# Kernel tuning notes

Measured on AMD Instinct MI355X. Metric: run time of the kernel, lower is better.

Reference implementation:

```python
import jax, jax.numpy as jnp
import numpy as np

WINDOW_SIZE = 7
L = 255.0
C1 = (0.01 * L) ** 2
C2 = (0.03 * L) ** 2


def _box_filter(x, window):
    # x: [B,1,H,W], window: [1,1,k,k] (uniform 1/k^2). VALID conv, groups=1.
    return jax.lax.conv_general_dilated(
        x, window, window_strides=(1, 1), padding='VALID',
        dimension_numbers=('NCHW', 'OIHW', 'NCHW'))


def setup_inputs() -> dict:
    key = jax.random.key(0)
    k1, k2 = jax.random.split(key)
    shape = (16, 1, 1080, 1920)
    img1 = jax.random.uniform(k1, shape, dtype=jnp.float32) * L
    img2 = jax.random.uniform(k2, shape, dtype=jnp.float32) * L
    window = jnp.ones((1, 1, WINDOW_SIZE, WINDOW_SIZE), dtype=jnp.float32) / (WINDOW_SIZE * WINDOW_SIZE)
    return {"img1": img1, "img2": img2, "window": window}


def reference(img1, img2, window):
    mu1 = _box_filter(img1, window)
    mu2 = _box_filter(img2, window)
    mu1_sq = mu1 * mu1
    mu2_sq = mu2 * mu2
    mu1_mu2 = mu1 * mu2
    sigma1_sq = _box_filter(img1 * img1, window) - mu1_sq
    sigma2_sq = _box_filter(img2 * img2, window) - mu2_sq
    sigma12 = _box_filter(img1 * img2, window) - mu1_mu2
    v1 = 2.0 * sigma12 + C2
    v2 = sigma1_sq + sigma2_sq + C2
    ssim_map = (2.0 * mu1_mu2 + C1) * v1 / ((mu1_sq + mu2_sq + C1) * v2)
    return jnp.mean(ssim_map)
```

## Files before the change

kernel.cpp:

```cpp
#include <hip/hip_runtime.h>


constexpr int W_IN = 1920;
constexpr int H_IN = 1080;
constexpr int WOUT = W_IN - 6;
constexpr int HOUT = H_IN - 6;
constexpr int NBATCH = 16;

constexpr int TW = 256;
constexpr int TH = 64;
constexpr int SROWS = 7;
constexpr int NSTAGES = 10;
constexpr int LSTRIDE = 264;
constexpr int C4_PER_ROW = 66;
constexpr int TASKS_PER_IMG = SROWS * C4_PER_ROW;
constexpr int TASKS = 2 * TASKS_PER_IMG;
constexpr int IMG_OFF = SROWS * LSTRIDE;
constexpr int BUF_OFF = 2 * IMG_OFF;

constexpr int NBX = 8, NBY = 17;
constexpr int NBLOCKS = NBX * NBY * NBATCH;

constexpr float C1f = 6.5025f;
constexpr float C2f = 58.5225f;
constexpr float INV49 = 1.0f / 49.0f;

__global__ __launch_bounds__(256)
void ssim_kernel(const float* __restrict__ img1, const float* __restrict__ img2,
                 double* __restrict__ partial) {
  const int tid = threadIdx.x;
  const int x0 = blockIdx.x * TW;
  const int y0 = blockIdx.y * TH;
  const size_t ibase = (size_t)blockIdx.z * (size_t)(H_IN * W_IN);
  const float* __restrict__ b1p = img1 + ibase;
  const float* __restrict__ b2p = img2 + ibase;

  __shared__ float sh[2 * BUF_OFF];
  __shared__ float warpsum[4];

#define DECODE(K)                                                        \
  const int  i##K  = tid + (K)*256;                                      \
  const bool v##K  = i##K < TASKS;                                       \
  const int  im##K = (i##K >= TASKS_PER_IMG) ? 1 : 0;                    \
  const int  rm##K = i##K - im##K * TASKS_PER_IMG;                       \
  const int  r##K  = rm##K / C4_PER_ROW;                                 \
  const int  c##K  = rm##K - r##K * C4_PER_ROW;                          \
  const int  gx##K = min(x0 + c##K * 4, W_IN - 4);                       \
  const float* pb##K = (im##K ? b2p : b1p) + gx##K;                      \
  const int  ld##K = (im##K * SROWS + r##K) * LSTRIDE + c##K * 4;
  DECODE(0) DECODE(1) DECODE(2) DECODE(3)
#undef DECODE

  float4 g0, g1, g2, g3;
#define GLOAD(K, ROW0)                                                   \
  if (v##K) {                                                            \
    const int gy = min(y0 + (ROW0) + r##K, H_IN - 1);                    \
    g##K = *reinterpret_cast<const float4*>(pb##K + (size_t)gy * W_IN);  \
  }
#define SWRITE(K, BUFBASE)                                               \
  if (v##K) *reinterpret_cast<float4*>(sh + (BUFBASE) + ld##K) = g##K;

#define DECL_SLOT(J) float h1_##J, h2_##J, h11_##J, h22_##J, h12_##J;
  DECL_SLOT(0) DECL_SLOT(1) DECL_SLOT(2) DECL_SLOT(3)
  DECL_SLOT(4) DECL_SLOT(5) DECL_SLOT(6)
#undef DECL_SLOT

  float accv = 0.0f;
  const bool colv = (x0 + tid) < WOUT;

  GLOAD(0, 0) GLOAD(1, 0) GLOAD(2, 0) GLOAD(3, 0)
  SWRITE(0, 0) SWRITE(1, 0) SWRITE(2, 0) SWRITE(3, 0)

  for (int s = 0; s < NSTAGES; ++s) {
    const int nrow0 = (s + 1) * SROWS;
    if (s + 1 < NSTAGES) {
      GLOAD(0, nrow0) GLOAD(1, nrow0) GLOAD(2, nrow0) GLOAD(3, nrow0)
    }
    __syncthreads();
    if (s + 1 < NSTAGES) {
      const int nb = ((s + 1) & 1) * BUF_OFF;
      SWRITE(0, nb) SWRITE(1, nb) SWRITE(2, nb) SWRITE(3, nb)
    }
    const float* rowbase = sh + (s & 1) * BUF_OFF + tid;

#define ROWSTEP(J)                                                           \
  {                                                                          \
    const float* ra = rowbase + (J) * LSTRIDE;                               \
    const float* rb = ra + IMG_OFF;                                          \
    float t1 = 0.f, t2 = 0.f, t11 = 0.f, t22 = 0.f, t12 = 0.f;               \
    _Pragma("unroll")                                                        \
    for (int d = 0; d < 7; ++d) {                                            \
      const float a = ra[d];                                                 \
      const float b = rb[d];                                                 \
      t1 += a; t2 += b;                                                      \
      t11 = fmaf(a, a, t11); t22 = fmaf(b, b, t22); t12 = fmaf(a, b, t12);   \
    }                                                                        \
    h1_##J = t1; h2_##J = t2; h11_##J = t11; h22_##J = t22; h12_##J = t12;   \
    const int ridx = s * SROWS + (J);                                        \
    if (ridx >= 6) {                                                         \
      const float bs1  = ((h1_0+h1_1)+(h1_2+h1_3))+((h1_4+h1_5)+h1_6);       \
      const float bs2  = ((h2_0+h2_1)+(h2_2+h2_3))+((h2_4+h2_5)+h2_6);       \
      const float bs11 = ((h11_0+h11_1)+(h11_2+h11_3))+((h11_4+h11_5)+h11_6);\
      const float bs22 = ((h22_0+h22_1)+(h22_2+h22_3))+((h22_4+h22_5)+h22_6);\
      const float bs12 = ((h12_0+h12_1)+(h12_2+h12_3))+((h12_4+h12_5)+h12_6);\
      const float mu1 = bs1 * INV49, mu2 = bs2 * INV49;                      \
      const float mu1s = mu1 * mu1, mu2s = mu2 * mu2, mu12 = mu1 * mu2;      \
      const float sg1  = fmaf(bs11, INV49, -mu1s);                           \
      const float sg2  = fmaf(bs22, INV49, -mu2s);                           \
      const float sg12 = fmaf(bs12, INV49, -mu12);                           \
      const float v1 = 2.0f * sg12 + C2f;                                    \
      const float v2 = sg1 + sg2 + C2f;                                      \
      const float num = (2.0f * mu12 + C1f) * v1;                            \
      const float den = (mu1s + mu2s + C1f) * v2;                            \
      const float ssim = num * __builtin_amdgcn_rcpf(den);                   \
      const int oy = y0 + ridx - 6;                                          \
      if (colv && oy < HOUT) accv += ssim;                                   \
    }                                                                        \
  }
    ROWSTEP(0) ROWSTEP(1) ROWSTEP(2) ROWSTEP(3)
    ROWSTEP(4) ROWSTEP(5) ROWSTEP(6)
#undef ROWSTEP
  }

#pragma unroll
  for (int off = 32; off > 0; off >>= 1) accv += __shfl_down(accv, off);
  if ((tid & 63) == 0) warpsum[tid >> 6] = accv;
  __syncthreads();
  if (tid == 0) {
    const double s = (double)warpsum[0] + (double)warpsum[1] +
                     (double)warpsum[2] + (double)warpsum[3];
    const int bid = blockIdx.x + NBX * (blockIdx.y + NBY * blockIdx.z);
    partial[bid] = s;
  }
}

__global__ __launch_bounds__(256)
void finalize_kernel(const double* __restrict__ partial,
                     float* __restrict__ out) {
  const int tid = threadIdx.x;
  double s = 0.0;
  for (int i = tid; i < NBLOCKS; i += 256) s += partial[i];
#pragma unroll
  for (int off = 32; off > 0; off >>= 1) s += __shfl_down(s, off);
  __shared__ double ws[4];
  if ((tid & 63) == 0) ws[tid >> 6] = s;
  __syncthreads();
  if (tid == 0) {
    const double tot = ws[0] + ws[1] + ws[2] + ws[3];
    out[0] = (float)(tot / ((double)NBATCH * (double)HOUT * (double)WOUT));
  }
}

extern "C" void kernel_launch(void* const* d_in, const int* in_sizes, int n_in,
                              void* d_out, int out_size, void* d_ws, size_t ws_size,
                              hipStream_t stream) {
  const float* img1 = (const float*)d_in[0];
  const float* img2 = (const float*)d_in[1];
  double* partial = (double*)d_ws;
  dim3 grid(NBX, NBY, NBATCH);
  hipLaunchKernelGGL(ssim_kernel, grid, dim3(256), 0, stream, img1, img2,
                     partial);
  hipLaunchKernelGGL(finalize_kernel, dim3(1), dim3(256), 0, stream, partial,
                     (float*)d_out);
}
```

Before: 300.7 us.

## Use sliding-window vertical sums with wide tiles and 9-slot row ring buffer

Replaces the per-output 7-row recomputation with a running vertical sum: each new row's horizontal sums are added and the row leaving the window is subtracted, using a 9-slot shared-memory ring of rows. Each thread now handles 4 adjacent columns, computing horizontal box sums with sliding add/subtract from float4 loads, and tiles widen to 1016 columns, which cuts halo reloads. Global loads are register-prefetched two rows ahead. The aim is fewer LDS reads and ALU ops per output. In exchange it adds a barrier per row, fewer blocks (544), and float cancellation error from the running add/subtract sums.

```diff
diff --git a/kernel.cpp b/kernel.cpp
--- a/kernel.cpp
+++ b/kernel.cpp
@@ -1,136 +1,186 @@
 #include <hip/hip_runtime.h>
 
 
-constexpr int W_IN = 1920;
-constexpr int H_IN = 1080;
+constexpr int W_IN = 1920, H_IN = 1080;
 constexpr int WOUT = W_IN - 6;
 constexpr int HOUT = H_IN - 6;
 constexpr int NBATCH = 16;
-
-constexpr int TW = 256;
+constexpr int TW = 1016;
 constexpr int TH = 64;
-constexpr int SROWS = 7;
-constexpr int NSTAGES = 10;
-constexpr int LSTRIDE = 264;
-constexpr int C4_PER_ROW = 66;
-constexpr int TASKS_PER_IMG = SROWS * C4_PER_ROW;
-constexpr int TASKS = 2 * TASKS_PER_IMG;
-constexpr int IMG_OFF = SROWS * LSTRIDE;
-constexpr int BUF_OFF = 2 * IMG_OFF;
-
-constexpr int NBX = 8, NBY = 17;
-constexpr int NBLOCKS = NBX * NBY * NBATCH;
+constexpr int NITER = TH + 6;
+constexpr int SLOTW = 1024;
+constexpr int NSLOT = 9;
+constexpr int NBX = 2, NBY = 17;
+constexpr int NBLK = NBX * NBY * NBATCH;
 
 constexpr float C1f = 6.5025f;
 constexpr float C2f = 58.5225f;
 constexpr float INV49 = 1.0f / 49.0f;
 
-__global__ __launch_bounds__(256)
+__global__ __launch_bounds__(256, 2)
 void ssim_kernel(const float* __restrict__ img1, const float* __restrict__ img2,
                  double* __restrict__ partial) {
-  const int tid = threadIdx.x;
+  const int t = threadIdx.x;
   const int x0 = blockIdx.x * TW;
   const int y0 = blockIdx.y * TH;
-  const size_t ibase = (size_t)blockIdx.z * (size_t)(H_IN * W_IN);
-  const float* __restrict__ b1p = img1 + ibase;
-  const float* __restrict__ b2p = img2 + ibase;
-
-  __shared__ float sh[2 * BUF_OFF];
-  __shared__ float warpsum[4];
-
-#define DECODE(K)                                                        \
-  const int  i##K  = tid + (K)*256;                                      \
-  const bool v##K  = i##K < TASKS;                                       \
-  const int  im##K = (i##K >= TASKS_PER_IMG) ? 1 : 0;                    \
-  const int  rm##K = i##K - im##K * TASKS_PER_IMG;                       \
-  const int  r##K  = rm##K / C4_PER_ROW;                                 \
-  const int  c##K  = rm##K - r##K * C4_PER_ROW;                          \
-  const int  gx##K = min(x0 + c##K * 4, W_IN - 4);                       \
-  const float* pb##K = (im##K ? b2p : b1p) + gx##K;                      \
-  const int  ld##K = (im##K * SROWS + r##K) * LSTRIDE + c##K * 4;
-  DECODE(0) DECODE(1) DECODE(2) DECODE(3)
-#undef DECODE
-
-  float4 g0, g1, g2, g3;
-#define GLOAD(K, ROW0)                                                   \
-  if (v##K) {                                                            \
-    const int gy = min(y0 + (ROW0) + r##K, H_IN - 1);                    \
-    g##K = *reinterpret_cast<const float4*>(pb##K + (size_t)gy * W_IN);  \
-  }
-#define SWRITE(K, BUFBASE)                                               \
-  if (v##K) *reinterpret_cast<float4*>(sh + (BUFBASE) + ld##K) = g##K;
-
-#define DECL_SLOT(J) float h1_##J, h2_##J, h11_##J, h22_##J, h12_##J;
-  DECL_SLOT(0) DECL_SLOT(1) DECL_SLOT(2) DECL_SLOT(3)
-  DECL_SLOT(4) DECL_SLOT(5) DECL_SLOT(6)
-#undef DECL_SLOT
-
-  float accv = 0.0f;
-  const bool colv = (x0 + tid) < WOUT;
-
-  GLOAD(0, 0) GLOAD(1, 0) GLOAD(2, 0) GLOAD(3, 0)
-  SWRITE(0, 0) SWRITE(1, 0) SWRITE(2, 0) SWRITE(3, 0)
-
-  for (int s = 0; s < NSTAGES; ++s) {
-    const int nrow0 = (s + 1) * SROWS;
-    if (s + 1 < NSTAGES) {
-      GLOAD(0, nrow0) GLOAD(1, nrow0) GLOAD(2, nrow0) GLOAD(3, nrow0)
-    }
-    __syncthreads();
-    if (s + 1 < NSTAGES) {
-      const int nb = ((s + 1) & 1) * BUF_OFF;
-      SWRITE(0, nb) SWRITE(1, nb) SWRITE(2, nb) SWRITE(3, nb)
-    }
-    const float* rowbase = sh + (s & 1) * BUF_OFF + tid;
-
-#define ROWSTEP(J)                                                           \
-  {                                                                          \
-    const float* ra = rowbase + (J) * LSTRIDE;                               \
-    const float* rb = ra + IMG_OFF;                                          \
-    float t1 = 0.f, t2 = 0.f, t11 = 0.f, t22 = 0.f, t12 = 0.f;               \
-    _Pragma("unroll")                                                        \
-    for (int d = 0; d < 7; ++d) {                                            \
-      const float a = ra[d];                                                 \
-      const float b = rb[d];                                                 \
-      t1 += a; t2 += b;                                                      \
-      t11 = fmaf(a, a, t11); t22 = fmaf(b, b, t22); t12 = fmaf(a, b, t12);   \
-    }                                                                        \
-    h1_##J = t1; h2_##J = t2; h11_##J = t11; h22_##J = t22; h12_##J = t12;   \
-    const int ridx = s * SROWS + (J);                                        \
-    if (ridx >= 6) {                                                         \
-      const float bs1  = ((h1_0+h1_1)+(h1_2+h1_3))+((h1_4+h1_5)+h1_6);       \
-      const float bs2  = ((h2_0+h2_1)+(h2_2+h2_3))+((h2_4+h2_5)+h2_6);       \
-      const float bs11 = ((h11_0+h11_1)+(h11_2+h11_3))+((h11_4+h11_5)+h11_6);\
-      const float bs22 = ((h22_0+h22_1)+(h22_2+h22_3))+((h22_4+h22_5)+h22_6);\
-      const float bs12 = ((h12_0+h12_1)+(h12_2+h12_3))+((h12_4+h12_5)+h12_6);\
-      const float mu1 = bs1 * INV49, mu2 = bs2 * INV49;                      \
-      const float mu1s = mu1 * mu1, mu2s = mu2 * mu2, mu12 = mu1 * mu2;      \
-      const float sg1  = fmaf(bs11, INV49, -mu1s);                           \
-      const float sg2  = fmaf(bs22, INV49, -mu2s);                           \
-      const float sg12 = fmaf(bs12, INV49, -mu12);                           \
-      const float v1 = 2.0f * sg12 + C2f;                                    \
-      const float v2 = sg1 + sg2 + C2f;                                      \
-      const float num = (2.0f * mu12 + C1f) * v1;                            \
-      const float den = (mu1s + mu2s + C1f) * v2;                            \
-      const float ssim = num * __builtin_amdgcn_rcpf(den);                   \
-      const int oy = y0 + ridx - 6;                                          \
-      if (colv && oy < HOUT) accv += ssim;                                   \
-    }                                                                        \
-  }
-    ROWSTEP(0) ROWSTEP(1) ROWSTEP(2) ROWSTEP(3)
-    ROWSTEP(4) ROWSTEP(5) ROWSTEP(6)
-#undef ROWSTEP
-  }
+  const size_t ib = (size_t)blockIdx.z * (size_t)(H_IN * W_IN);
+  const float* __restrict__ p1 = img1 + ib;
+  const float* __restrict__ p2 = img2 + ib;
+
+  __shared__ float sh[NSLOT][2][SLOTW];
+  __shared__ float wsum[4];
+
+  const int lc = 4 * t;
+  const int gcol = min(x0 + lc, W_IN - 4);
+  const int rdo = min(lc, SLOTW - 12);
+  const int ldso = lc;
+
+  const bool m0 = (lc + 0 < TW) && (x0 + lc + 0 < WOUT);
+  const bool m1 = (lc + 1 < TW) && (x0 + lc + 1 < WOUT);
+  const bool m2 = (lc + 2 < TW) && (x0 + lc + 2 < WOUT);
+  const bool m3 = (lc + 3 < TW) && (x0 + lc + 3 < WOUT);
+
+  float V1_0 = 0.f, V1_1 = 0.f, V1_2 = 0.f, V1_3 = 0.f;
+  float V2_0 = 0.f, V2_1 = 0.f, V2_2 = 0.f, V2_3 = 0.f;
+  float V11_0 = 0.f, V11_1 = 0.f, V11_2 = 0.f, V11_3 = 0.f;
+  float V22_0 = 0.f, V22_1 = 0.f, V22_2 = 0.f, V22_3 = 0.f;
+  float V12_0 = 0.f, V12_1 = 0.f, V12_2 = 0.f, V12_3 = 0.f;
+  float accv = 0.f;
+
+  {
+    const int gy = min(y0, H_IN - 1);
+    const float4 a = *(const float4*)(p1 + (size_t)gy * W_IN + gcol);
+    const float4 b = *(const float4*)(p2 + (size_t)gy * W_IN + gcol);
+    *(float4*)&sh[0][0][ldso] = a;
+    *(float4*)&sh[0][1][ldso] = b;
+  }
+  float4 Aa, Ab, Ba, Bb;
+  {
+    const int gy = min(y0 + 1, H_IN - 1);
+    Aa = *(const float4*)(p1 + (size_t)gy * W_IN + gcol);
+    Ab = *(const float4*)(p2 + (size_t)gy * W_IN + gcol);
+  }
+  {
+    const int gy = min(y0 + 2, H_IN - 1);
+    Ba = *(const float4*)(p1 + (size_t)gy * W_IN + gcol);
+    Bb = *(const float4*)(p2 + (size_t)gy * W_IN + gcol);
+  }
+
+  int sw = 1, sn = 0, so = 2;
+  int gyld = min(y0 + 3, H_IN - 1);
+  int oy = y0;
+
+#define ADV(x) x = ((x) == NSLOT - 1) ? 0 : (x) + 1
+
+#define HPASS(SLOT, OP)                                                       \
+  {                                                                           \
+    const float* _pa = &sh[SLOT][0][rdo];                                     \
+    const float* _pb = &sh[SLOT][1][rdo];                                     \
+    const float4 _a0 = *(const float4*)(_pa);                                 \
+    const float4 _a1 = *(const float4*)(_pa + 4);                             \
+    const float4 _a2 = *(const float4*)(_pa + 8);                             \
+    const float4 _b0 = *(const float4*)(_pb);                                 \
+    const float4 _b1 = *(const float4*)(_pb + 4);                             \
+    const float4 _b2 = *(const float4*)(_pb + 8);                             \
+    float s;                                                                  \
+    s = ((_a0.x + _a0.y) + (_a0.z + _a0.w)) + ((_a1.x + _a1.y) + _a1.z);      \
+    V1_0 OP s;                                                                \
+    s = s - _a0.x + _a1.w;  V1_1 OP s;                                        \
+    s = s - _a0.y + _a2.x;  V1_2 OP s;                                        \
+    s = s - _a0.z + _a2.y;  V1_3 OP s;                                        \
+    s = ((_b0.x + _b0.y) + (_b0.z + _b0.w)) + ((_b1.x + _b1.y) + _b1.z);      \
+    V2_0 OP s;                                                                \
+    s = s - _b0.x + _b1.w;  V2_1 OP s;                                        \
+    s = s - _b0.y + _b2.x;  V2_2 OP s;                                        \
+    s = s - _b0.z + _b2.y;  V2_3 OP s;                                        \
+    s = _a0.x * _a0.x;                                                        \
+    s = fmaf(_a0.y, _a0.y, s); s = fmaf(_a0.z, _a0.z, s);                     \
+    s = fmaf(_a0.w, _a0.w, s); s = fmaf(_a1.x, _a1.x, s);                     \
+    s = fmaf(_a1.y, _a1.y, s); s = fmaf(_a1.z, _a1.z, s);                     \
+    V11_0 OP s;                                                               \
+    s = fmaf(-_a0.x, _a0.x, fmaf(_a1.w, _a1.w, s));  V11_1 OP s;              \
+    s = fmaf(-_a0.y, _a0.y, fmaf(_a2.x, _a2.x, s));  V11_2 OP s;              \
+    s = fmaf(-_a0.z, _a0.z, fmaf(_a2.y, _a2.y, s));  V11_3 OP s;              \
+    s = _b0.x * _b0.x;                                                        \
+    s = fmaf(_b0.y, _b0.y, s); s = fmaf(_b0.z, _b0.z, s);                     \
+    s = fmaf(_b0.w, _b0.w, s); s = fmaf(_b1.x, _b1.x, s);                     \
+    s = fmaf(_b1.y, _b1.y, s); s = fmaf(_b1.z, _b1.z, s);                     \
+    V22_0 OP s;                                                               \
+    s = fmaf(-_b0.x, _b0.x, fmaf(_b1.w, _b1.w, s));  V22_1 OP s;              \
+    s = fmaf(-_b0.y, _b0.y, fmaf(_b2.x, _b2.x, s));  V22_2 OP s;              \
+    s = fmaf(-_b0.z, _b0.z, fmaf(_b2.y, _b2.y, s));  V22_3 OP s;              \
+    s = _a0.x * _b0.x;                                                        \
+    s = fmaf(_a0.y, _b0.y, s); s = fmaf(_a0.z, _b0.z, s);                     \
+    s = fmaf(_a0.w, _b0.w, s); s = fmaf(_a1.x, _b1.x, s);                     \
+    s = fmaf(_a1.y, _b1.y, s); s = fmaf(_a1.z, _b1.z, s);                     \
+    V12_0 OP s;                                                               \
+    s = fmaf(-_a0.x, _b0.x, fmaf(_a1.w, _b1.w, s));  V12_1 OP s;              \
+    s = fmaf(-_a0.y, _b0.y, fmaf(_a2.x, _b2.x, s));  V12_2 OP s;              \
+    s = fmaf(-_a0.z, _b0.z, fmaf(_a2.y, _b2.y, s));  V12_3 OP s;              \
+  }
+
+#define EPI1(VA, VB, VAA, VBB, VAB, MASK)                                     \
+  {                                                                           \
+    const float mu1 = (VA) * INV49, mu2 = (VB) * INV49;                       \
+    const float mu1s = mu1 * mu1, mu2s = mu2 * mu2, mu12 = mu1 * mu2;         \
+    const float sg1 = fmaf((VAA), INV49, -mu1s);                              \
+    const float sg2 = fmaf((VBB), INV49, -mu2s);                              \
+    const float sg12 = fmaf((VAB), INV49, -mu12);                             \
+    const float v1 = fmaf(2.f, sg12, C2f);                                    \
+    const float v2 = sg1 + sg2 + C2f;                                         \
+    const float num = fmaf(2.f, mu12, C1f) * v1;                              \
+    const float den = (mu1s + mu2s + C1f) * v2;                               \
+    const float ss = num * __builtin_amdgcn_rcpf(den);                        \
+    accv += (MASK) ? ss : 0.f;                                                \
+  }
+
+#define BODY(RA, RB, DO_OLD, DO_EPI)                                          \
+  {                                                                           \
+    __syncthreads();                                                          \
+    *(float4*)&sh[sw][0][ldso] = RA;                                          \
+    *(float4*)&sh[sw][1][ldso] = RB;                                          \
+    RA = *(const float4*)(p1 + (size_t)gyld * W_IN + gcol);                   \
+    RB = *(const float4*)(p2 + (size_t)gyld * W_IN + gcol);                   \
+    gyld = min(gyld + 1, H_IN - 1);                                           \
+    HPASS(sn, +=)                                                             \
+    if (DO_OLD) { HPASS(so, -=) }                                             \
+    if (DO_EPI) {                                                             \
+      if (oy < HOUT) {                                                        \
+        EPI1(V1_0, V2_0, V11_0, V22_0, V12_0, m0)                             \
+        EPI1(V1_1, V2_1, V11_1, V22_1, V12_1, m1)                             \
+        EPI1(V1_2, V2_2, V11_2, V22_2, V12_2, m2)                             \
+        EPI1(V1_3, V2_3, V11_3, V22_3, V12_3, m3)                             \
+      }                                                                       \
+      ++oy;                                                                   \
+    }                                                                         \
+    ADV(sw); ADV(sn); ADV(so);                                                \
+  }
+
+  BODY(Aa, Ab, false, false)
+  BODY(Ba, Bb, false, false)
+  BODY(Aa, Ab, false, false)
+  BODY(Ba, Bb, false, false)
+  BODY(Aa, Ab, false, false)
+  BODY(Ba, Bb, false, false)
+  BODY(Aa, Ab, false, true)
+  BODY(Ba, Bb, true,  true)
+  for (int k = 8; k < NITER; k += 2) {
+    BODY(Aa, Ab, true, true)
+    BODY(Ba, Bb, true, true)
+  }
+#undef BODY
+#undef HPASS
+#undef EPI1
+#undef ADV
 
 #pragma unroll
   for (int off = 32; off > 0; off >>= 1) accv += __shfl_down(accv, off);
-  if ((tid & 63) == 0) warpsum[tid >> 6] = accv;
+  if ((t & 63) == 0) wsum[t >> 6] = accv;
   __syncthreads();
-  if (tid == 0) {
-    const double s = (double)warpsum[0] + (double)warpsum[1] +
-                     (double)warpsum[2] + (double)warpsum[3];
+  if (t == 0) {
     const int bid = blockIdx.x + NBX * (blockIdx.y + NBY * blockIdx.z);
-    partial[bid] = s;
+    partial[bid] = (double)wsum[0] + (double)wsum[1] +
+                   (double)wsum[2] + (double)wsum[3];
   }
 }
 
@@ -139,7 +189,7 @@
                      float* __restrict__ out) {
   const int tid = threadIdx.x;
   double s = 0.0;
-  for (int i = tid; i < NBLOCKS; i += 256) s += partial[i];
+  for (int i = tid; i < NBLK; i += 256) s += partial[i];
 #pragma unroll
   for (int off = 32; off > 0; off >>= 1) s += __shfl_down(s, off);
   __shared__ double ws[4];
```

Result: slower. 325.9 us (+8.4%).

## Use 4-column-per-thread wide tiles with sliding-window running sums

Applied to the files above, without the earlier changes.

Restructures the SSIM kernel so each thread handles four adjacent output columns across a 1016-wide tile and streams rows one at a time through a double-buffered shared row. Horizontal sums are computed incrementally across the four columns and vertical sums via running sums with a 7-row ring in registers, replacing full 7x7 recomputation. The aim is to cut redundant ALU and LDS reads and the halo overhead of the smaller 256x64 tiles. In exchange it uses many registers, syncs once per row, and launches far fewer blocks (512), which may limit occupancy and latency hiding. Running-sum subtraction also adds float rounding drift.

```diff
diff --git a/kernel.cpp b/kernel.cpp
--- a/kernel.cpp
+++ b/kernel.cpp
@@ -1,136 +1,173 @@
 #include <hip/hip_runtime.h>
 
 
-constexpr int W_IN = 1920;
-constexpr int H_IN = 1080;
+constexpr int W_IN = 1920, H_IN = 1080;
 constexpr int WOUT = W_IN - 6;
 constexpr int HOUT = H_IN - 6;
 constexpr int NBATCH = 16;
-
-constexpr int TW = 256;
-constexpr int TH = 64;
-constexpr int SROWS = 7;
-constexpr int NSTAGES = 10;
-constexpr int LSTRIDE = 264;
-constexpr int C4_PER_ROW = 66;
-constexpr int TASKS_PER_IMG = SROWS * C4_PER_ROW;
-constexpr int TASKS = 2 * TASKS_PER_IMG;
-constexpr int IMG_OFF = SROWS * LSTRIDE;
-constexpr int BUF_OFF = 2 * IMG_OFF;
-
-constexpr int NBX = 8, NBY = 17;
-constexpr int NBLOCKS = NBX * NBY * NBATCH;
+constexpr int TW = 1016;
+constexpr int TH = 71;
+constexpr int NITER = 77;
+constexpr int SLOTW = 1024;
+constexpr int NBX = 2, NBY = 16;
+constexpr int NBLK = NBX * NBY * NBATCH;
 
 constexpr float C1f = 6.5025f;
 constexpr float C2f = 58.5225f;
 constexpr float INV49 = 1.0f / 49.0f;
 
-__global__ __launch_bounds__(256)
+__global__ __launch_bounds__(256, 2)
 void ssim_kernel(const float* __restrict__ img1, const float* __restrict__ img2,
                  double* __restrict__ partial) {
-  const int tid = threadIdx.x;
+  const int t = threadIdx.x;
   const int x0 = blockIdx.x * TW;
   const int y0 = blockIdx.y * TH;
-  const size_t ibase = (size_t)blockIdx.z * (size_t)(H_IN * W_IN);
-  const float* __restrict__ b1p = img1 + ibase;
-  const float* __restrict__ b2p = img2 + ibase;
-
-  __shared__ float sh[2 * BUF_OFF];
-  __shared__ float warpsum[4];
-
-#define DECODE(K)                                                        \
-  const int  i##K  = tid + (K)*256;                                      \
-  const bool v##K  = i##K < TASKS;                                       \
-  const int  im##K = (i##K >= TASKS_PER_IMG) ? 1 : 0;                    \
-  const int  rm##K = i##K - im##K * TASKS_PER_IMG;                       \
-  const int  r##K  = rm##K / C4_PER_ROW;                                 \
-  const int  c##K  = rm##K - r##K * C4_PER_ROW;                          \
-  const int  gx##K = min(x0 + c##K * 4, W_IN - 4);                       \
-  const float* pb##K = (im##K ? b2p : b1p) + gx##K;                      \
-  const int  ld##K = (im##K * SROWS + r##K) * LSTRIDE + c##K * 4;
-  DECODE(0) DECODE(1) DECODE(2) DECODE(3)
-#undef DECODE
-
-  float4 g0, g1, g2, g3;
-#define GLOAD(K, ROW0)                                                   \
-  if (v##K) {                                                            \
-    const int gy = min(y0 + (ROW0) + r##K, H_IN - 1);                    \
-    g##K = *reinterpret_cast<const float4*>(pb##K + (size_t)gy * W_IN);  \
-  }
-#define SWRITE(K, BUFBASE)                                               \
-  if (v##K) *reinterpret_cast<float4*>(sh + (BUFBASE) + ld##K) = g##K;
-
-#define DECL_SLOT(J) float h1_##J, h2_##J, h11_##J, h22_##J, h12_##J;
-  DECL_SLOT(0) DECL_SLOT(1) DECL_SLOT(2) DECL_SLOT(3)
-  DECL_SLOT(4) DECL_SLOT(5) DECL_SLOT(6)
-#undef DECL_SLOT
-
-  float accv = 0.0f;
-  const bool colv = (x0 + tid) < WOUT;
-
-  GLOAD(0, 0) GLOAD(1, 0) GLOAD(2, 0) GLOAD(3, 0)
-  SWRITE(0, 0) SWRITE(1, 0) SWRITE(2, 0) SWRITE(3, 0)
-
-  for (int s = 0; s < NSTAGES; ++s) {
-    const int nrow0 = (s + 1) * SROWS;
-    if (s + 1 < NSTAGES) {
-      GLOAD(0, nrow0) GLOAD(1, nrow0) GLOAD(2, nrow0) GLOAD(3, nrow0)
-    }
-    __syncthreads();
-    if (s + 1 < NSTAGES) {
-      const int nb = ((s + 1) & 1) * BUF_OFF;
-      SWRITE(0, nb) SWRITE(1, nb) SWRITE(2, nb) SWRITE(3, nb)
-    }
-    const float* rowbase = sh + (s & 1) * BUF_OFF + tid;
-
-#define ROWSTEP(J)                                                           \
+  const size_t ib = (size_t)blockIdx.z * (size_t)(H_IN * W_IN);
+  const float* __restrict__ p1 = img1 + ib;
+  const float* __restrict__ p2 = img2 + ib;
+
+  __shared__ float sh[2][2][SLOTW];
+  __shared__ float wsum[4];
+
+  const int lc = 4 * t;
+  const int gcol = min(x0 + lc, W_IN - 4);
+  const int rdo = min(lc, SLOTW - 12);
+
+  const bool m0 = (lc + 0 < TW) && (x0 + lc + 0 < WOUT);
+  const bool m1 = (lc + 1 < TW) && (x0 + lc + 1 < WOUT);
+  const bool m2 = (lc + 2 < TW) && (x0 + lc + 2 < WOUT);
+  const bool m3 = (lc + 3 < TW) && (x0 + lc + 3 < WOUT);
+
+#define DECLR(Q, C)                                                          \
+  float R##Q##_##C##_0 = 0.f, R##Q##_##C##_1 = 0.f, R##Q##_##C##_2 = 0.f,    \
+        R##Q##_##C##_3 = 0.f, R##Q##_##C##_4 = 0.f, R##Q##_##C##_5 = 0.f,    \
+        R##Q##_##C##_6 = 0.f;
+  DECLR(1, 0) DECLR(1, 1) DECLR(1, 2) DECLR(1, 3)
+  DECLR(2, 0) DECLR(2, 1) DECLR(2, 2) DECLR(2, 3)
+  DECLR(3, 0) DECLR(3, 1) DECLR(3, 2) DECLR(3, 3)
+  DECLR(4, 0) DECLR(4, 1) DECLR(4, 2) DECLR(4, 3)
+  DECLR(5, 0) DECLR(5, 1) DECLR(5, 2) DECLR(5, 3)
+#undef DECLR
+#define DECLV(Q) float V##Q##_0 = 0.f, V##Q##_1 = 0.f, V##Q##_2 = 0.f, V##Q##_3 = 0.f;
+  DECLV(1) DECLV(2) DECLV(3) DECLV(4) DECLV(5)
+#undef DECLV
+
+  float accv = 0.f;
+
+  {
+    const float4 a = *(const float4*)(p1 + (size_t)min(y0, H_IN - 1) * W_IN + gcol);
+    const float4 b = *(const float4*)(p2 + (size_t)min(y0, H_IN - 1) * W_IN + gcol);
+    *(float4*)&sh[0][0][lc] = a;
+    *(float4*)&sh[0][1][lc] = b;
+  }
+  float4 RA = *(const float4*)(p1 + (size_t)min(y0 + 1, H_IN - 1) * W_IN + gcol);
+  float4 RB = *(const float4*)(p2 + (size_t)min(y0 + 1, H_IN - 1) * W_IN + gcol);
+  int gyld = min(y0 + 2, H_IN - 1);
+  int oy = y0;
+
+#define QC(Q, C, J)                                                          \
+  { V##Q##_##C += s - R##Q##_##C##_##J; R##Q##_##C##_##J = s; }
+
+#define EPI1(VA, VB, VAA, VBB, VAB, MASK)                                    \
   {                                                                          \
-    const float* ra = rowbase + (J) * LSTRIDE;                               \
-    const float* rb = ra + IMG_OFF;                                          \
-    float t1 = 0.f, t2 = 0.f, t11 = 0.f, t22 = 0.f, t12 = 0.f;               \
-    _Pragma("unroll")                                                        \
-    for (int d = 0; d < 7; ++d) {                                            \
-      const float a = ra[d];                                                 \
-      const float b = rb[d];                                                 \
-      t1 += a; t2 += b;                                                      \
-      t11 = fmaf(a, a, t11); t22 = fmaf(b, b, t22); t12 = fmaf(a, b, t12);   \
+    const float mu1 = (VA) * INV49, mu2 = (VB) * INV49;                      \
+    const float mu1s = mu1 * mu1, mu2s = mu2 * mu2, mu12 = mu1 * mu2;        \
+    const float sg1 = fmaf((VAA), INV49, -mu1s);                             \
+    const float sg2 = fmaf((VBB), INV49, -mu2s);                             \
+    const float sg12 = fmaf((VAB), INV49, -mu12);                            \
+    const float v1 = fmaf(2.f, sg12, C2f);                                   \
+    const float v2 = sg1 + sg2 + C2f;                                        \
+    const float num = fmaf(2.f, mu12, C1f) * v1;                             \
+    const float den = (mu1s + mu2s + C1f) * v2;                              \
+    const float ss = num * __builtin_amdgcn_rcpf(den);                       \
+    accv += (MASK) ? ss : 0.f;                                               \
+  }
+
+#define STEP(J, WS, RS, DO_EPI)                                              \
+  {                                                                          \
+    __syncthreads();                                                         \
+    *(float4*)&sh[WS][0][lc] = RA;                                           \
+    *(float4*)&sh[WS][1][lc] = RB;                                           \
+    RA = *(const float4*)(p1 + (size_t)gyld * W_IN + gcol);                  \
+    RB = *(const float4*)(p2 + (size_t)gyld * W_IN + gcol);                  \
+    gyld = min(gyld + 1, H_IN - 1);                                          \
+    const float* _pa = &sh[RS][0][rdo];                                      \
+    const float* _pb = &sh[RS][1][rdo];                                      \
+    const float4 a0 = *(const float4*)(_pa);                                 \
+    const float4 a1 = *(const float4*)(_pa + 4);                             \
+    const float4 a2 = *(const float4*)(_pa + 8);                             \
+    const float4 b0 = *(const float4*)(_pb);                                 \
+    const float4 b1 = *(const float4*)(_pb + 4);                             \
+    const float4 b2 = *(const float4*)(_pb + 8);                             \
+    float s;                                                                 \
+    s = ((a0.x + a0.y) + (a0.z + a0.w)) + ((a1.x + a1.y) + a1.z);            \
+    QC(1, 0, J)                                                              \
+    s = s - a0.x + a1.w;  QC(1, 1, J)                                        \
+    s = s - a0.y + a2.x;  QC(1, 2, J)                                        \
+    s = s - a0.z + a2.y;  QC(1, 3, J)                                        \
+    s = ((b0.x + b0.y) + (b0.z + b0.w)) + ((b1.x + b1.y) + b1.z);            \
+    QC(2, 0, J)                                                              \
+    s = s - b0.x + b1.w;  QC(2, 1, J)                                        \
+    s = s - b0.y + b2.x;  QC(2, 2, J)                                        \
+    s = s - b0.z + b2.y;  QC(2, 3, J)                                        \
+    s = a0.x * a0.x;                                                         \
+    s = fmaf(a0.y, a0.y, s); s = fmaf(a0.z, a0.z, s);                        \
+    s = fmaf(a0.w, a0.w, s); s = fmaf(a1.x, a1.x, s);                        \
+    s = fmaf(a1.y, a1.y, s); s = fmaf(a1.z, a1.z, s);                        \
+    QC(3, 0, J)                                                              \
+    s = fmaf(-a0.x, a0.x, fmaf(a1.w, a1.w, s));  QC(3, 1, J)                 \
+    s = fmaf(-a0.y, a0.y, fmaf(a2.x, a2.x, s));  QC(3, 2, J)                 \
+    s = fmaf(-a0.z, a0.z, fmaf(a2.y, a2.y, s));  QC(3, 3, J)                 \
+    s = b0.x * b0.x;                                                         \
+    s = fmaf(b0.y, b0.y, s); s = fmaf(b0.z, b0.z, s);                        \
+    s = fmaf(b0.w, b0.w, s); s = fmaf(b1.x, b1.x, s);                        \
+    s = fmaf(b1.y, b1.y, s); s = fmaf(b1.z, b1.z, s);                        \
+    QC(4, 0, J)                                                              \
+    s = fmaf(-b0.x, b0.x, fmaf(b1.w, b1.w, s));  QC(4, 1, J)                 \
+    s = fmaf(-b0.y, b0.y, fmaf(b2.x, b2.x, s));  QC(4, 2, J)                 \
+    s = fmaf(-b0.z, b0.z, fmaf(b2.y, b2.y, s));  QC(4, 3, J)                 \
+    s = a0.x * b0.x;                                                         \
+    s = fmaf(a0.y, b0.y, s); s = fmaf(a0.z, b0.z, s);                        \
+    s = fmaf(a0.w, b0.w, s); s = fmaf(a1.x, b1.x, s);                        \
+    s = fmaf(a1.y, b1.y, s); s = fmaf(a1.z, b1.z, s);                        \
+    QC(5, 0, J)                                                              \
+    s = fmaf(-a0.x, b0.x, fmaf(a1.w, b1.w, s));  QC(5, 1, J)                 \
+    s = fmaf(-a0.y, b0.y, fmaf(a2.x, b2.x, s));  QC(5, 2, J)                 \
+    s = fmaf(-a0.z, b0.z, fmaf(a2.y, b2.y, s));  QC(5, 3, J)                 \
+    if (DO_EPI) {                                                            \
+      if (oy < HOUT) {                                                       \
+        EPI1(V1_0, V2_0, V3_0, V4_0, V5_0, m0)                               \
+        EPI1(V1_1, V2_1, V3_1, V4_1, V5_1, m1)                               \
+        EPI1(V1_2, V2_2, V3_2, V4_2, V5_2, m2)                               \
+        EPI1(V1_3, V2_3, V3_3, V4_3, V5_3, m3)                               \
+      }                                                                      \
+      ++oy;                                                                  \
     }                                                                        \
-    h1_##J = t1; h2_##J = t2; h11_##J = t11; h22_##J = t22; h12_##J = t12;   \
-    const int ridx = s * SROWS + (J);                                        \
-    if (ridx >= 6) {                                                         \
-      const float bs1  = ((h1_0+h1_1)+(h1_2+h1_3))+((h1_4+h1_5)+h1_6);       \
-      const float bs2  = ((h2_0+h2_1)+(h2_2+h2_3))+((h2_4+h2_5)+h2_6);       \
-      const float bs11 = ((h11_0+h11_1)+(h11_2+h11_3))+((h11_4+h11_5)+h11_6);\
-      const float bs22 = ((h22_0+h22_1)+(h22_2+h22_3))+((h22_4+h22_5)+h22_6);\
-      const float bs12 = ((h12_0+h12_1)+(h12_2+h12_3))+((h12_4+h12_5)+h12_6);\
-      const float mu1 = bs1 * INV49, mu2 = bs2 * INV49;                      \
-      const float mu1s = mu1 * mu1, mu2s = mu2 * mu2, mu12 = mu1 * mu2;      \
-      const float sg1  = fmaf(bs11, INV49, -mu1s);                           \
-      const float sg2  = fmaf(bs22, INV49, -mu2s);                           \
-      const float sg12 = fmaf(bs12, INV49, -mu12);                           \
-      const float v1 = 2.0f * sg12 + C2f;                                    \
-      const float v2 = sg1 + sg2 + C2f;                                      \
-      const float num = (2.0f * mu12 + C1f) * v1;                            \
-      const float den = (mu1s + mu2s + C1f) * v2;                            \
-      const float ssim = num * __builtin_amdgcn_rcpf(den);                   \
-      const int oy = y0 + ridx - 6;                                          \
-      if (colv && oy < HOUT) accv += ssim;                                   \
-    }                                                                        \
-  }
-    ROWSTEP(0) ROWSTEP(1) ROWSTEP(2) ROWSTEP(3)
-    ROWSTEP(4) ROWSTEP(5) ROWSTEP(6)
-#undef ROWSTEP
-  }
+  }
+
+  STEP(0, 1, 0, false) STEP(1, 0, 1, false) STEP(2, 1, 0, false)
+  STEP(3, 0, 1, false) STEP(4, 1, 0, false) STEP(5, 0, 1, false)
+  STEP(6, 1, 0, true)
+  for (int gp = 0; gp < 5; ++gp) {
+    STEP(0, 0, 1, true) STEP(1, 1, 0, true) STEP(2, 0, 1, true)
+    STEP(3, 1, 0, true) STEP(4, 0, 1, true) STEP(5, 1, 0, true)
+    STEP(6, 0, 1, true)
+    STEP(0, 1, 0, true) STEP(1, 0, 1, true) STEP(2, 1, 0, true)
+    STEP(3, 0, 1, true) STEP(4, 1, 0, true) STEP(5, 0, 1, true)
+    STEP(6, 1, 0, true)
+  }
+#undef STEP
+#undef QC
+#undef EPI1
 
 #pragma unroll
   for (int off = 32; off > 0; off >>= 1) accv += __shfl_down(accv, off);
-  if ((tid & 63) == 0) warpsum[tid >> 6] = accv;
+  if ((t & 63) == 0) wsum[t >> 6] = accv;
   __syncthreads();
-  if (tid == 0) {
-    const double s = (double)warpsum[0] + (double)warpsum[1] +
-                     (double)warpsum[2] + (double)warpsum[3];
+  if (t == 0) {
     const int bid = blockIdx.x + NBX * (blockIdx.y + NBY * blockIdx.z);
-    partial[bid] = s;
+    partial[bid] = (double)wsum[0] + (double)wsum[1] +
+                   (double)wsum[2] + (double)wsum[3];
   }
 }
 
@@ -139,7 +176,7 @@
                      float* __restrict__ out) {
   const int tid = threadIdx.x;
   double s = 0.0;
-  for (int i = tid; i < NBLOCKS; i += 256) s += partial[i];
+  for (int i = tid; i < NBLK; i += 256) s += partial[i];
 #pragma unroll
   for (int off = 32; off > 0; off >>= 1) s += __shfl_down(s, off);
   __shared__ double ws[4];
```

New measurement: 312.6 us. 4.0% more time.
